# Kernel tuning notes

Hardware: AMD Instinct MI355X
Metric: run time of the kernel (lower is better)

## Reference

```python
import jax, jax.numpy as jnp
import numpy as np

B, C, H, W = 4, 192, 128, 128
NH = 6
HD = C // NH            # 32
GS = 8                  # window (group) size
K = 16                  # unfold kernel size
STRIDE, PAD = 8, 4
NUM = H // GS           # 16 groups per side
BG = B * NUM * NUM      # 1024 windows
N = GS * GS             # 64 tokens per group
KK = K * K              # 256 sampled tokens per window
SCALE = HD ** -0.5


def _rope(x):
    # lucidrains-style rotary embedding along dim -2 (positions), last dim = head_dim
    d = x.shape[-1]
    inv = 1.0 / (10000.0 ** (jnp.arange(0, d, 2, dtype=jnp.float32) / d))
    t = jnp.arange(x.shape[-2], dtype=jnp.float32)
    freqs = jnp.repeat(t[:, None] * inv[None, :], 2, axis=-1)  # [seq, d], interleaved
    cos, sin = jnp.cos(freqs), jnp.sin(freqs)
    xp = x.reshape(x.shape[:-1] + (d // 2, 2))
    xr = jnp.stack((-xp[..., 1], xp[..., 0]), axis=-1).reshape(x.shape)
    return x * cos + xr * sin


def _l2norm(x):
    # torch F.normalize(dim=-1): x / max(||x||, eps)
    n = jnp.linalg.norm(x, axis=-1, keepdims=True)
    return x / jnp.maximum(n, 1e-12)


def setup_inputs() -> dict:
    key = jax.random.key(0)
    ks = jax.random.split(key, 6)
    return {
        "x_complete": jax.random.normal(ks[0], (B, C, H, W), jnp.float32),
        "graph": jax.random.randint(ks[1], (BG, 1, N, KK), 0, 2) > 0,
        "w_group": jax.random.normal(ks[2], (C, C), jnp.float32) * 0.02,
        "b_group": jnp.zeros((C,), jnp.float32),
        "w_sample": jax.random.normal(ks[3], (2 * C, C), jnp.float32) * 0.02,
        "b_sample": jnp.zeros((2 * C,), jnp.float32),
        "w_proj": jax.random.normal(ks[4], (C, C), jnp.float32) * 0.02,
        "b_proj": jnp.zeros((C,), jnp.float32),
    }


def reference(x_complete, graph, w_group, b_group, w_sample, b_sample, w_proj, b_proj):
    # --- local grouping: [B,C,(numh sh),(numw sw)] -> [(B numh numw), sh*sw, C]
    xg = x_complete.reshape(B, C, NUM, GS, NUM, GS).transpose(0, 2, 4, 3, 5, 1).reshape(BG, N, C)
    # --- proj_group: 1x1 Conv1d over channels, then split heads 'b (h c) n -> b h n c'
    x1 = jnp.einsum('bnc,dc->bnd', xg, w_group) + b_group
    x1 = x1.reshape(BG, N, NH, HD).transpose(0, 2, 1, 3)            # [BG,NH,N,HD]
    # --- proj_sample: 1x1 Conv2d to 2C channels
    xs = jnp.einsum('bchw,dc->bdhw', x_complete, w_sample) + b_sample[None, :, None, None]
    # --- F.unfold(kernel=16, stride=8, pad=4): patch features channel-major (c,k0,k1)
    patches = jax.lax.conv_general_dilated_patches(
        xs, (K, K), (STRIDE, STRIDE), ((PAD, PAD), (PAD, PAD)))    # [B, 2C*KK, NUM, NUM]
    xs = patches.reshape(B, 2 * C, KK, NUM * NUM).transpose(0, 3, 2, 1).reshape(BG, KK, 2 * C)
    # --- 'b n (div h c) -> div b h n c'
    xs = xs.reshape(BG, KK, 2, NH, HD)
    x2 = xs[:, :, 0].transpose(0, 2, 1, 3)                          # [BG,NH,KK,HD]
    feat = xs[:, :, 1].transpose(0, 2, 1, 3)                        # [BG,NH,KK,HD]
    # --- RoPE + masked cosine-sim attention
    q = _rope(x1)
    k = _rope(x2)
    sim = jnp.einsum('bhmc,bhnc->bhmn', _l2norm(q), _l2norm(k))
    sim = sim + (-100.0) * (~graph).astype(sim.dtype)
    corr = jax.nn.softmax(sim * SCALE, axis=-1)                     # [BG,NH,N,KK]
    out = jnp.einsum('bhmn,bhnc->bhmc', corr, feat)                 # [BG,NH,N,HD]
    out = out.transpose(0, 2, 1, 3).reshape(BG, N, C)
    return out @ w_proj.T + b_proj
```

## Files before the change

kernel.cpp:

```cpp
#include <hip/hip_runtime.h>
#include <hip/hip_bf16.h>

#define B_    4
#define C_    192
#define C2_   384
#define PIX_  16384
#define NH_   6
#define BG_   1024
#define SCALE_ 0.17677669529663687f
#define C1_ 0.2550348943f

typedef __attribute__((ext_vector_type(8))) short short8v;
typedef __attribute__((ext_vector_type(4))) float f32x4;

__global__ __launch_bounds__(256, 1)
void k_rope_init(float2* __restrict__ tbl) {
    int e = blockIdx.x * 256 + threadIdx.x;
    if (e >= 4096) return;
    int pos = e >> 4, j = e & 15;
    float freq = powf(10.0f, -0.25f * (float)j);
    float ang = (float)pos * freq;
    float sn, cs;
    sincosf(ang, &sn, &cs);
    tbl[e] = make_float2(cs, sn);
}

__global__ __launch_bounds__(256, 4)
void k_gmask(const int* __restrict__ g, unsigned int* __restrict__ gbits) {
    int e = blockIdx.x * 256 + threadIdx.x;
    const uint4* p = (const uint4*)(g + (size_t)e * 32);
    unsigned int m = 0u;
#pragma unroll
    for (int i = 0; i < 8; ++i) {
        uint4 v = p[i];
        m |= (v.x ? 1u : 0u) << (i * 4);
        m |= (v.y ? 1u : 0u) << (i * 4 + 1);
        m |= (v.z ? 1u : 0u) << (i * 4 + 2);
        m |= (v.w ? 1u : 0u) << (i * 4 + 3);
    }
    gbits[e] = m;
}

__global__ __launch_bounds__(256, 4)
void k_wcast(const float* __restrict__ wsm, const float* __restrict__ wgb,
             const float* __restrict__ wpj, __hip_bfloat16* __restrict__ wb)
{
    int e = (blockIdx.x * 256 + threadIdx.x) * 4;
    float4 v = (e < 73728) ? *(const float4*)(wsm + e)
             : (e < 110592) ? *(const float4*)(wgb + (e - 73728))
                            : *(const float4*)(wpj + (e - 110592));
    union { uint2 u; __hip_bfloat16 h[4]; } pk;
    pk.h[0] = __float2bfloat16(v.x); pk.h[1] = __float2bfloat16(v.y);
    pk.h[2] = __float2bfloat16(v.z); pk.h[3] = __float2bfloat16(v.w);
    *(uint2*)(wb + e) = pk.u;
}

__global__ __launch_bounds__(256, 4)
void k_convm(const float* __restrict__ x, const __hip_bfloat16* __restrict__ wb,
             const float* __restrict__ bsm, const float* __restrict__ bgb,
             const float2* __restrict__ tbl,
             __hip_bfloat16* __restrict__ xsk, __hip_bfloat16* __restrict__ xsv,
             __hip_bfloat16* __restrict__ qbf)
{
    __shared__ __align__(16) char smem[25600];
    const int bid = blockIdx.x;
    const int b = bid >> 8, pt = bid & 255;
    const int px0 = pt * 64;
    const int t = threadIdx.x;

    {
        const int px = t & 63, cq = t >> 6;
        const float* src = x + ((size_t)b * C_ + cq * 48) * PIX_ + px0 + px;
        char* row = smem + px * 400 + cq * 96;
#pragma unroll
        for (int i = 0; i < 6; ++i) {
            union { uint4 u; __hip_bfloat16 h[8]; } pk;
#pragma unroll
            for (int j = 0; j < 8; ++j)
                pk.h[j] = __float2bfloat16(src[(size_t)(i * 8 + j) * PIX_]);
            *(uint4*)(row + i * 16) = pk.u;
        }
    }
    __syncthreads();

    const int w = t >> 6, lane = t & 63;
    const int l15 = lane & 15, g = lane >> 4;
    const int mb = (w & 1) * 32;
    const int nb = (w >> 1) * 32;

    short8v a0r[6], a1r[6];
#pragma unroll
    for (int ks = 0; ks < 6; ++ks) {
        a0r[ks] = *(const short8v*)(smem + (mb + l15) * 400      + ks * 64 + g * 16);
        a1r[ks] = *(const short8v*)(smem + (mb + 16 + l15) * 400 + ks * 64 + g * 16);
    }
    __syncthreads();

    float* ot = (float*)smem;
    const f32x4 zz = {0.0f, 0.0f, 0.0f, 0.0f};

    for (int oct = 0; oct < 9; ++oct) {
        f32x4 acc00 = zz, acc01 = zz, acc10 = zz, acc11 = zz;
        const __hip_bfloat16* w0 = wb + (size_t)(oct * 64 + nb + l15) * C_;
        const __hip_bfloat16* w1 = w0 + 16 * C_;
#pragma unroll
        for (int ks = 0; ks < 6; ++ks) {
            const short8v b0 = *(const short8v*)(w0 + ks * 32 + g * 8);
            const short8v b1 = *(const short8v*)(w1 + ks * 32 + g * 8);
            acc00 = __builtin_amdgcn_mfma_f32_16x16x32_bf16(a0r[ks], b0, acc00, 0, 0, 0);
            acc01 = __builtin_amdgcn_mfma_f32_16x16x32_bf16(a0r[ks], b1, acc01, 0, 0, 0);
            acc10 = __builtin_amdgcn_mfma_f32_16x16x32_bf16(a1r[ks], b0, acc10, 0, 0, 0);
            acc11 = __builtin_amdgcn_mfma_f32_16x16x32_bf16(a1r[ks], b1, acc11, 0, 0, 0);
        }
        __syncthreads();

        if (oct >= 3 && oct < 6) {
            *(f32x4*)&ot[(nb + l15) * 68      + mb + g * 4]      = acc00;
            *(f32x4*)&ot[(nb + l15) * 68      + mb + 16 + g * 4] = acc10;
            *(f32x4*)&ot[(nb + 16 + l15) * 68 + mb + g * 4]      = acc01;
            *(f32x4*)&ot[(nb + 16 + l15) * 68 + mb + 16 + g * 4] = acc11;
        } else {
#pragma unroll
            for (int j = 0; j < 4; ++j) {
                ot[(mb + g * 4 + j) * 68      + nb + l15]      = acc00[j];
                ot[(mb + 16 + g * 4 + j) * 68 + nb + l15]      = acc10[j];
                ot[(mb + g * 4 + j) * 68      + nb + 16 + l15] = acc01[j];
                ot[(mb + 16 + g * 4 + j) * 68 + nb + 16 + l15] = acc11[j];
            }
        }
        __syncthreads();

        if (oct < 3) {
            const int px = t >> 2, i = t & 3;
            const int ocb = oct * 64 + i * 16;
            float v[16];
#pragma unroll
            for (int q4 = 0; q4 < 4; ++q4) {
                float4 vv = *(const float4*)&ot[px * 68 + i * 16 + q4 * 4];
                float4 bv = *(const float4*)(bsm + ocb + q4 * 4);
                v[q4 * 4 + 0] = vv.x + bv.x; v[q4 * 4 + 1] = vv.y + bv.y;
                v[q4 * 4 + 2] = vv.z + bv.z; v[q4 * 4 + 3] = vv.w + bv.w;
            }
            float n2 = 0.0f;
#pragma unroll
            for (int d = 0; d < 16; ++d) n2 = fmaf(v[d], v[d], n2);
            n2 += __shfl_xor(n2, 1);
            const float inv = 1.0f / fmaxf(sqrtf(n2), 1e-12f);
            union { uint4 u[2]; __hip_bfloat16 h[16]; } pk;
#pragma unroll
            for (int d = 0; d < 16; ++d) pk.h[d] = __float2bfloat16(v[d] * inv);
            __hip_bfloat16* dst = xsk + ((size_t)b * PIX_ + px0 + px) * C_ + ocb;
            *(uint4*)dst       = pk.u[0];
            *(uint4*)(dst + 8) = pk.u[1];
        } else if (oct < 6) {
            const float* bias = bsm + oct * 64;
#pragma unroll
            for (int e0 = 0; e0 < 2; ++e0) {
                const int e = e0 * 256 + t;
                const int oc = e >> 3, seg = e & 7;
                const float bo = bias[oc];
                float4 v0 = *(const float4*)&ot[oc * 68 + seg * 8];
                float4 v1 = *(const float4*)&ot[oc * 68 + seg * 8 + 4];
                union { uint4 u; __hip_bfloat16 h[8]; } pk;
                pk.h[0] = __float2bfloat16(v0.x + bo); pk.h[1] = __float2bfloat16(v0.y + bo);
                pk.h[2] = __float2bfloat16(v0.z + bo); pk.h[3] = __float2bfloat16(v0.w + bo);
                pk.h[4] = __float2bfloat16(v1.x + bo); pk.h[5] = __float2bfloat16(v1.y + bo);
                pk.h[6] = __float2bfloat16(v1.z + bo); pk.h[7] = __float2bfloat16(v1.w + bo);
                *(uint4*)(xsv + (size_t)(b * C_ + (oct - 3) * 64 + oc) * PIX_ + px0 + seg * 8) = pk.u;
            }
        } else {
            const int px = t & 63, hh = t >> 6;
            if (hh < 2) {
                const int p = px0 + px;
                const int r = p >> 7, c = p & 127;
                const int n = (r & 7) * 8 + (c & 7);
                const int bg = (b << 8) + ((r >> 3) << 4) + (c >> 3);
                const int hglob = (oct - 6) * 2 + hh;
                float v[32];
#pragma unroll
                for (int d4 = 0; d4 < 8; ++d4) {
                    float4 vv = *(const float4*)&ot[px * 68 + hh * 32 + d4 * 4];
                    float4 bv = *(const float4*)(bgb + hglob * 32 + d4 * 4);
                    v[d4 * 4 + 0] = vv.x + bv.x; v[d4 * 4 + 1] = vv.y + bv.y;
                    v[d4 * 4 + 2] = vv.z + bv.z; v[d4 * 4 + 3] = vv.w + bv.w;
                }
                float rr[32];
#pragma unroll
                for (int j = 0; j < 16; ++j) {
                    float2 cs = tbl[n * 16 + j];
                    float a0 = v[2 * j], a1 = v[2 * j + 1];
                    rr[2 * j]     = a0 * cs.x - a1 * cs.y;
                    rr[2 * j + 1] = a1 * cs.x + a0 * cs.y;
                }
                float n2 = 0.0f;
#pragma unroll
                for (int d = 0; d < 32; ++d) n2 = fmaf(rr[d], rr[d], n2);
                const float inv = 1.0f / fmaxf(sqrtf(n2), 1e-12f);
                __hip_bfloat16* dst = qbf + ((size_t)(bg * NH_ + hglob) * 64 + n) * 32;
#pragma unroll
                for (int c8 = 0; c8 < 4; ++c8) {
                    union { uint4 u; __hip_bfloat16 h[8]; } pk;
#pragma unroll
                    for (int i = 0; i < 8; ++i) pk.h[i] = __float2bfloat16(rr[c8 * 8 + i] * inv);
                    *(uint4*)(dst + c8 * 8) = pk.u;
                }
            }
        }
    }
}

__global__ __launch_bounds__(512, 2)
void k_attn(const __hip_bfloat16* __restrict__ xsk, const __hip_bfloat16* __restrict__ xsv,
            const unsigned int* __restrict__ gbits, const __hip_bfloat16* __restrict__ qb,
            const float2* __restrict__ tbl, float* __restrict__ attn)
{
    __shared__ __align__(16) char smem[52736];
    const int bid0 = blockIdx.x;
    const int bid = (bid0 & 7) * 768 + (bid0 >> 3);
    const int h = bid % NH_;
    const int bg = bid / NH_;
    const int b = bg >> 8, ph = (bg >> 4) & 15, pw = bg & 15;
    const int t = threadIdx.x;
    const int w = t >> 6, lane = t & 63;
    const int g = lane >> 4, l15 = lane & 15;
    const int rbase = (w & 3) * 16;
    const int wcol  = w >> 2;
    const int cb    = wcol * 128;
    const int cb32  = wcol * 4;

    const short8v qa = *(const short8v*)(qb +
        ((size_t)(bg * NH_ + h) * 64 + rbase + l15) * 32 + g * 8);

    {
        const int m = t >> 1, half = t & 1;
        const int k0 = m >> 4, k1 = m & 15;
        const int rr = ph * 8 - 4 + k0, cc = pw * 8 - 4 + k1;
        const bool inb = ((unsigned)rr < 128u) && ((unsigned)cc < 128u);
        float kv[16];
        if (inb) {
            const uint4* pk = (const uint4*)(xsk +
                ((size_t)b * PIX_ + rr * 128 + cc) * C_ + h * 32 + half * 16);
            union { uint4 u; __hip_bfloat16 h8[8]; } r0, r1;
            r0.u = pk[0]; r1.u = pk[1];
#pragma unroll
            for (int d = 0; d < 8; ++d) {
                kv[d]     = __bfloat162float(r0.h8[d]);
                kv[8 + d] = __bfloat162float(r1.h8[d]);
            }
        } else {
#pragma unroll
            for (int d = 0; d < 16; ++d) kv[d] = 0.0f;
        }
        union { uint4 u; __hip_bfloat16 hh[8]; } p0, p1;
#pragma unroll
        for (int p = 0; p < 8; ++p) {
            float2 cs = tbl[m * 16 + half * 8 + p];
            float a0 = kv[2 * p], a1 = kv[2 * p + 1];
            float e0 = a0 * cs.x - a1 * cs.y;
            float e1 = a1 * cs.x + a0 * cs.y;
            if (p < 4) { p0.hh[2 * p] = __float2bfloat16(e0); p0.hh[2 * p + 1] = __float2bfloat16(e1); }
            else { p1.hh[2 * (p - 4)] = __float2bfloat16(e0); p1.hh[2 * (p - 4) + 1] = __float2bfloat16(e1); }
        }
        *(uint4*)(smem + m * 80 + half * 32)      = p0.u;
        *(uint4*)(smem + m * 80 + half * 32 + 16) = p1.u;
    }

    {
        const int d = t & 31, k0 = t >> 5;
        const int rr = ph * 8 - 4 + k0;
        const int c0 = pw * 8 - 4;
        char* dst = smem + 34816 + d * 528 + k0 * 32;
        const __hip_bfloat16* src = xsv + (size_t)(b * C_ + h * 32 + d) * PIX_ + rr * 128 + c0;
        const bool rok = (unsigned)rr < 128u;
        if (rok && pw >= 1 && pw <= 14) {
            const uint2* s2 = (const uint2*)src;
            uint2 a0 = s2[0], a1 = s2[1], a2 = s2[2], a3 = s2[3];
            ((uint4*)dst)[0] = make_uint4(a0.x, a0.y, a1.x, a1.y);
            ((uint4*)dst)[1] = make_uint4(a2.x, a2.y, a3.x, a3.y);
        } else {
            __hip_bfloat16* dh = (__hip_bfloat16*)dst;
            __hip_bfloat16 z = __float2bfloat16(0.0f);
#pragma unroll
            for (int i = 0; i < 16; ++i) {
                bool ok = rok && ((unsigned)(c0 + i) < 128u);
                dh[i] = ok ? src[i] : z;
            }
        }
    }

    {
        unsigned int* gbl = (unsigned int*)(smem + 20480);
        const int q = t >> 3, wd = t & 7;
        gbl[q * 9 + wd] = gbits[(size_t)bg * 512 + t];
    }
    __syncthreads();

    f32x4 acc[8];
    const f32x4 zz = {0.0f, 0.0f, 0.0f, 0.0f};
#pragma unroll
    for (int tile = 0; tile < 8; ++tile) {
        const short8v kb = *(const short8v*)(smem + (cb + tile * 16 + l15) * 80 + g * 16);
        acc[tile] = __builtin_amdgcn_mfma_f32_16x16x32_bf16(qa, kb, zz, 0, 0, 0);
    }

    const unsigned int* gbl = (const unsigned int*)(smem + 20480);
    float* reds = (float*)(smem + 51712);
    float sm4[4], inv4[4];
#pragma unroll
    for (int j = 0; j < 4; ++j) {
        const int q = rbase + g * 4 + j;
        const unsigned int wv[4] = { gbl[q * 9 + cb32], gbl[q * 9 + cb32 + 1],
                                     gbl[q * 9 + cb32 + 2], gbl[q * 9 + cb32 + 3] };
        float sm = 0.0f;
#pragma unroll
        for (int tile = 0; tile < 8; ++tile) {
            const unsigned int bit = (wv[tile >> 1] >> ((tile & 1) * 16 + l15)) & 1u;
            float e = __builtin_amdgcn_exp2f(fmaf(acc[tile][j], C1_, -C1_));
            e = bit ? e : 0.0f;
            acc[tile][j] = e;
            sm += e;
        }
        sm += __shfl_xor(sm, 1);
        sm += __shfl_xor(sm, 2);
        sm += __shfl_xor(sm, 4);
        sm += __shfl_xor(sm, 8);
        sm4[j] = sm;
        if (l15 == 0) reds[wcol * 64 + q] = sm;
    }
    __syncthreads();
#pragma unroll
    for (int j = 0; j < 4; ++j) {
        const int q = rbase + g * 4 + j;
        inv4[j] = 1.0f / (sm4[j] + reds[(wcol ^ 1) * 64 + q] + 1e-37f);
    }

    char* plw = smem + w * 4352;
#pragma unroll
    for (int tile = 0; tile < 8; ++tile)
#pragma unroll
        for (int j = 0; j < 4; ++j) {
            *(__hip_bfloat16*)(plw + (g * 4 + j) * 272 + (tile * 16 + l15) * 2) =
                __float2bfloat16(acc[tile][j]);
        }

    f32x4 o0 = zz, o1 = zz;
#pragma unroll
    for (int ks = 0; ks < 4; ++ks) {
        const short8v pa  = *(const short8v*)(plw + l15 * 272 + (ks * 32 + g * 8) * 2);
        const short8v vb0 = *(const short8v*)(smem + 34816 + l15 * 528        + (cb + ks * 32 + g * 8) * 2);
        const short8v vb1 = *(const short8v*)(smem + 34816 + (16 + l15) * 528 + (cb + ks * 32 + g * 8) * 2);
        o0 = __builtin_amdgcn_mfma_f32_16x16x32_bf16(pa, vb0, o0, 0, 0, 0);
        o1 = __builtin_amdgcn_mfma_f32_16x16x32_bf16(pa, vb1, o1, 0, 0, 0);
    }
    __syncthreads();

    float* ob = (float*)smem;
    if (wcol == 1) {
#pragma unroll
        for (int j = 0; j < 4; ++j) {
            const int q = rbase + g * 4 + j;
            ob[q * 33 + l15]      = o0[j];
            ob[q * 33 + 16 + l15] = o1[j];
        }
    }
    __syncthreads();
    if (wcol == 0) {
#pragma unroll
        for (int j = 0; j < 4; ++j) {
            const int q = rbase + g * 4 + j;
            float v0 = (o0[j] + ob[q * 33 + l15])      * inv4[j];
            float v1 = (o1[j] + ob[q * 33 + 16 + l15]) * inv4[j];
            attn[((size_t)bg * 64 + q) * 192 + h * 32 + l15]      = v0;
            attn[((size_t)bg * 64 + q) * 192 + h * 32 + 16 + l15] = v1;
        }
    }
}

__global__ __launch_bounds__(256, 4)
void k_oprojm(const float* __restrict__ attn, const __hip_bfloat16* __restrict__ wpb,
              const float* __restrict__ bp, float* __restrict__ out)
{
    __shared__ __align__(16) char smem[25600];
    const int bid0 = blockIdx.x;
    const int bid = (bid0 & 7) * 384 + (bid0 >> 3);
    const int oct = bid % 3;
    const int rt  = bid / 3;
    const int row0 = rt * 64;
    const int t = threadIdx.x;

#pragma unroll
    for (int e0 = 0; e0 < 12; ++e0) {
        const int e = e0 * 256 + t;
        const int r = e / 48, c4 = e % 48;
        float4 v = *(const float4*)(attn + (size_t)(row0 + r) * 192 + c4 * 4);
        union { uint2 u; __hip_bfloat16 h[4]; } pk;
        pk.h[0] = __float2bfloat16(v.x); pk.h[1] = __float2bfloat16(v.y);
        pk.h[2] = __float2bfloat16(v.z); pk.h[3] = __float2bfloat16(v.w);
        *(uint2*)(smem + r * 400 + c4 * 8) = pk.u;
    }
    __syncthreads();

    const int w = t >> 6, lane = t & 63;
    const int l15 = lane & 15, g = lane >> 4;
    const int mb = (w & 1) * 32;
    const int nb = (w >> 1) * 32;

    const f32x4 zz = {0.0f, 0.0f, 0.0f, 0.0f};
    f32x4 acc00 = zz, acc01 = zz, acc10 = zz, acc11 = zz;
    const __hip_bfloat16* w0 = wpb + (size_t)(oct * 64 + nb + l15) * C_;
    const __hip_bfloat16* w1 = w0 + 16 * C_;
#pragma unroll
    for (int ks = 0; ks < 6; ++ks) {
        const short8v a0 = *(const short8v*)(smem + (mb + l15) * 400      + ks * 64 + g * 16);
        const short8v a1 = *(const short8v*)(smem + (mb + 16 + l15) * 400 + ks * 64 + g * 16);
        const short8v b0 = *(const short8v*)(w0 + ks * 32 + g * 8);
        const short8v b1 = *(const short8v*)(w1 + ks * 32 + g * 8);
        acc00 = __builtin_amdgcn_mfma_f32_16x16x32_bf16(a0, b0, acc00, 0, 0, 0);
        acc01 = __builtin_amdgcn_mfma_f32_16x16x32_bf16(a0, b1, acc01, 0, 0, 0);
        acc10 = __builtin_amdgcn_mfma_f32_16x16x32_bf16(a1, b0, acc10, 0, 0, 0);
        acc11 = __builtin_amdgcn_mfma_f32_16x16x32_bf16(a1, b1, acc11, 0, 0, 0);
    }
    __syncthreads();

    float* ot = (float*)smem;
#pragma unroll
    for (int j = 0; j < 4; ++j) {
        ot[(mb + g * 4 + j) * 68      + nb + l15]      = acc00[j];
        ot[(mb + 16 + g * 4 + j) * 68 + nb + l15]      = acc10[j];
        ot[(mb + g * 4 + j) * 68      + nb + 16 + l15] = acc01[j];
        ot[(mb + 16 + g * 4 + j) * 68 + nb + 16 + l15] = acc11[j];
    }
    __syncthreads();

    {
        const int k = t & 15, pxi = t >> 4;
        const float4 bias4 = *(const float4*)(bp + oct * 64 + k * 4);
#pragma unroll
        for (int p = 0; p < 4; ++p) {
            const int px = p * 16 + pxi;
            float4 v = *(const float4*)&ot[px * 68 + k * 4];
            v.x += bias4.x; v.y += bias4.y; v.z += bias4.z; v.w += bias4.w;
            *(float4*)(out + (size_t)(row0 + px) * 192 + oct * 64 + k * 4) = v;
        }
    }
}

extern "C" void kernel_launch(void* const* d_in, const int* in_sizes, int n_in,
                              void* d_out, int out_size, void* d_ws, size_t ws_size,
                              hipStream_t stream)
{
    (void)in_sizes; (void)n_in; (void)out_size; (void)ws_size;
    const float* x   = (const float*)d_in[0];
    const int* grph  = (const int*)d_in[1];
    const float* wg  = (const float*)d_in[2];
    const float* bgb = (const float*)d_in[3];
    const float* wsm = (const float*)d_in[4];
    const float* bsm = (const float*)d_in[5];
    const float* wp  = (const float*)d_in[6];
    const float* bp  = (const float*)d_in[7];
    float* out = (float*)d_out;

    char* wsb = (char*)d_ws;
    __hip_bfloat16* xsk = (__hip_bfloat16*)wsb;
    __hip_bfloat16* xsv = (__hip_bfloat16*)(wsb + 25165824ull);
    __hip_bfloat16* qbf = (__hip_bfloat16*)(wsb + 50331648ull);
    float2* tbl = (float2*)(wsb + 75497472ull);
    unsigned int* gbits = (unsigned int*)(wsb + 75530240ull);
    __hip_bfloat16* wb  = (__hip_bfloat16*)(wsb + 77627392ull);
    __hip_bfloat16* wpb = wb + 110592;

    hipLaunchKernelGGL(k_rope_init, dim3(16),   dim3(256), 0, stream, tbl);
    hipLaunchKernelGGL(k_wcast,     dim3(144),  dim3(256), 0, stream, wsm, wg, wp, wb);
    hipLaunchKernelGGL(k_gmask,     dim3(2048), dim3(256), 0, stream, grph, gbits);
    hipLaunchKernelGGL(k_convm,     dim3(1024), dim3(256), 0, stream, x, wb, bsm, bgb, tbl, xsk, xsv, qbf);
    hipLaunchKernelGGL(k_attn,      dim3(6144), dim3(512), 0, stream, xsk, xsv, gbits, qbf, tbl, out);
    hipLaunchKernelGGL(k_oprojm,    dim3(3072), dim3(256), 0, stream, out, wpb, bp, out);
}
```

Measured before the change: 196.7 us.

## Split conv projection kernel into three output groups per pixel tile

The fused 1x1 projection kernel now launches three blocks per 64-pixel tile, each computing one third of the output channels (key, value, or query group), instead of one block looping over all nine octets. The value group writes bf16 results directly from MFMA registers to global memory without the LDS transpose round-trip. Block IDs are remapped with an XCD-style interleave. The intent is more parallelism and less serial work per block, at the cost of reloading and converting the input tile three times.

```diff
diff --git a/kernel.cpp b/kernel.cpp
--- a/kernel.cpp
+++ b/kernel.cpp
@@ -63,8 +63,11 @@
              __hip_bfloat16* __restrict__ qbf)
 {
     __shared__ __align__(16) char smem[25600];
-    const int bid = blockIdx.x;
-    const int b = bid >> 8, pt = bid & 255;
+    const int bid0 = blockIdx.x;
+    const int bid = (bid0 & 7) * 384 + (bid0 >> 3);
+    const int ogrp = bid % 3;
+    const int pb   = bid / 3;
+    const int b = pb >> 8, pt = pb & 255;
     const int px0 = pt * 64;
     const int t = threadIdx.x;
 
@@ -94,12 +97,51 @@
         a0r[ks] = *(const short8v*)(smem + (mb + l15) * 400      + ks * 64 + g * 16);
         a1r[ks] = *(const short8v*)(smem + (mb + 16 + l15) * 400 + ks * 64 + g * 16);
     }
-    __syncthreads();
 
     float* ot = (float*)smem;
     const f32x4 zz = {0.0f, 0.0f, 0.0f, 0.0f};
 
-    for (int oct = 0; oct < 9; ++oct) {
+    if (ogrp == 1) {
+#pragma unroll
+        for (int o2 = 0; o2 < 3; ++o2) {
+            const int oct = 3 + o2;
+            f32x4 acc00 = zz, acc01 = zz, acc10 = zz, acc11 = zz;
+            const __hip_bfloat16* w0 = wb + (size_t)(oct * 64 + nb + l15) * C_;
+            const __hip_bfloat16* w1 = w0 + 16 * C_;
+#pragma unroll
+            for (int ks = 0; ks < 6; ++ks) {
+                const short8v b0 = *(const short8v*)(w0 + ks * 32 + g * 8);
+                const short8v b1 = *(const short8v*)(w1 + ks * 32 + g * 8);
+                acc00 = __builtin_amdgcn_mfma_f32_16x16x32_bf16(a0r[ks], b0, acc00, 0, 0, 0);
+                acc01 = __builtin_amdgcn_mfma_f32_16x16x32_bf16(a0r[ks], b1, acc01, 0, 0, 0);
+                acc10 = __builtin_amdgcn_mfma_f32_16x16x32_bf16(a1r[ks], b0, acc10, 0, 0, 0);
+                acc11 = __builtin_amdgcn_mfma_f32_16x16x32_bf16(a1r[ks], b1, acc11, 0, 0, 0);
+            }
+            const float bo0 = bsm[oct * 64 + nb + l15];
+            const float bo1 = bsm[oct * 64 + nb + 16 + l15];
+            union { uint2 u; __hip_bfloat16 h[4]; } p00, p10, p01, p11;
+#pragma unroll
+            for (int j = 0; j < 4; ++j) {
+                p00.h[j] = __float2bfloat16(acc00[j] + bo0);
+                p10.h[j] = __float2bfloat16(acc10[j] + bo0);
+                p01.h[j] = __float2bfloat16(acc01[j] + bo1);
+                p11.h[j] = __float2bfloat16(acc11[j] + bo1);
+            }
+            __hip_bfloat16* d0 = xsv + (size_t)(b * C_ + o2 * 64 + nb + l15) * PIX_
+                                     + px0 + mb + g * 4;
+            *(uint2*)d0        = p00.u;
+            *(uint2*)(d0 + 16) = p10.u;
+            __hip_bfloat16* d1 = d0 + (size_t)16 * PIX_;
+            *(uint2*)d1        = p01.u;
+            *(uint2*)(d1 + 16) = p11.u;
+        }
+        return;
+    }
+
+    __syncthreads();
+
+    for (int o2 = 0; o2 < 3; ++o2) {
+        const int oct = (ogrp == 0) ? o2 : 6 + o2;
         f32x4 acc00 = zz, acc01 = zz, acc10 = zz, acc11 = zz;
         const __hip_bfloat16* w0 = wb + (size_t)(oct * 64 + nb + l15) * C_;
         const __hip_bfloat16* w1 = w0 + 16 * C_;
@@ -114,23 +156,16 @@
         }
         __syncthreads();
 
-        if (oct >= 3 && oct < 6) {
-            *(f32x4*)&ot[(nb + l15) * 68      + mb + g * 4]      = acc00;
-            *(f32x4*)&ot[(nb + l15) * 68      + mb + 16 + g * 4] = acc10;
-            *(f32x4*)&ot[(nb + 16 + l15) * 68 + mb + g * 4]      = acc01;
-            *(f32x4*)&ot[(nb + 16 + l15) * 68 + mb + 16 + g * 4] = acc11;
-        } else {
-#pragma unroll
-            for (int j = 0; j < 4; ++j) {
-                ot[(mb + g * 4 + j) * 68      + nb + l15]      = acc00[j];
-                ot[(mb + 16 + g * 4 + j) * 68 + nb + l15]      = acc10[j];
-                ot[(mb + g * 4 + j) * 68      + nb + 16 + l15] = acc01[j];
-                ot[(mb + 16 + g * 4 + j) * 68 + nb + 16 + l15] = acc11[j];
-            }
+#pragma unroll
+        for (int j = 0; j < 4; ++j) {
+            ot[(mb + g * 4 + j) * 68      + nb + l15]      = acc00[j];
+            ot[(mb + 16 + g * 4 + j) * 68 + nb + l15]      = acc10[j];
+            ot[(mb + g * 4 + j) * 68      + nb + 16 + l15] = acc01[j];
+            ot[(mb + 16 + g * 4 + j) * 68 + nb + 16 + l15] = acc11[j];
         }
         __syncthreads();
 
-        if (oct < 3) {
+        if (ogrp == 0) {
             const int px = t >> 2, i = t & 3;
             const int ocb = oct * 64 + i * 16;
             float v[16];
@@ -152,22 +187,6 @@
             __hip_bfloat16* dst = xsk + ((size_t)b * PIX_ + px0 + px) * C_ + ocb;
             *(uint4*)dst       = pk.u[0];
             *(uint4*)(dst + 8) = pk.u[1];
-        } else if (oct < 6) {
-            const float* bias = bsm + oct * 64;
-#pragma unroll
-            for (int e0 = 0; e0 < 2; ++e0) {
-                const int e = e0 * 256 + t;
-                const int oc = e >> 3, seg = e & 7;
-                const float bo = bias[oc];
-                float4 v0 = *(const float4*)&ot[oc * 68 + seg * 8];
-                float4 v1 = *(const float4*)&ot[oc * 68 + seg * 8 + 4];
-                union { uint4 u; __hip_bfloat16 h[8]; } pk;
-                pk.h[0] = __float2bfloat16(v0.x + bo); pk.h[1] = __float2bfloat16(v0.y + bo);
-                pk.h[2] = __float2bfloat16(v0.z + bo); pk.h[3] = __float2bfloat16(v0.w + bo);
-                pk.h[4] = __float2bfloat16(v1.x + bo); pk.h[5] = __float2bfloat16(v1.y + bo);
-                pk.h[6] = __float2bfloat16(v1.z + bo); pk.h[7] = __float2bfloat16(v1.w + bo);
-                *(uint4*)(xsv + (size_t)(b * C_ + (oct - 3) * 64 + oc) * PIX_ + px0 + seg * 8) = pk.u;
-            }
         } else {
             const int px = t & 63, hh = t >> 6;
             if (hh < 2) {
@@ -472,7 +491,7 @@
     hipLaunchKernelGGL(k_rope_init, dim3(16),   dim3(256), 0, stream, tbl);
     hipLaunchKernelGGL(k_wcast,     dim3(144),  dim3(256), 0, stream, wsm, wg, wp, wb);
     hipLaunchKernelGGL(k_gmask,     dim3(2048), dim3(256), 0, stream, grph, gbits);
-    hipLaunchKernelGGL(k_convm,     dim3(1024), dim3(256), 0, stream, x, wb, bsm, bgb, tbl, xsk, xsv, qbf);
+    hipLaunchKernelGGL(k_convm,     dim3(3072), dim3(256), 0, stream, x, wb, bsm, bgb, tbl, xsk, xsv, qbf);
     hipLaunchKernelGGL(k_attn,      dim3(6144), dim3(512), 0, stream, xsk, xsv, gbits, qbf, tbl, out);
     hipLaunchKernelGGL(k_oprojm,    dim3(3072), dim3(256), 0, stream, out, wpb, bp, out);
 }
```

After: 205.0 us. 4.2% more time.
